# Performance work log

Measured on AMD Instinct MI355X. Metric: run time of the kernel, lower is better.

## Reference

```python
import jax, jax.numpy as jnp
import numpy as np

B, C, H, W = 4, 256, 64, 64
C8 = C // 8  # q/k projection dim = 32

def setup_inputs() -> dict:
    key = jax.random.key(0)
    ks = jax.random.split(key, 6)
    s = 0.02
    return {
        "x": jax.random.normal(ks[0], (B, C, H, W), dtype=jnp.float32),
        "wq": jax.random.normal(ks[1], (C8, C), dtype=jnp.float32) * s,
        "bq": jnp.zeros((C8,), dtype=jnp.float32),
        "wk": jax.random.normal(ks[2], (C8, C), dtype=jnp.float32) * s,
        "bk": jnp.zeros((C8,), dtype=jnp.float32),
        "wv": jax.random.normal(ks[3], (C, C), dtype=jnp.float32) * s,
        "bv": jnp.zeros((C,), dtype=jnp.float32),
        "wo": jax.random.normal(ks[4], (C, C), dtype=jnp.float32) * s,
        "bo": jnp.zeros((C,), dtype=jnp.float32),
        "scale": jnp.zeros((1,), dtype=jnp.float32),
    }

def reference(x, wq, bq, wk, bk, wv, bv, wo, bo, scale):
    b, c, h, w = x.shape
    n = h * w
    xf = x.reshape(b, c, n)  # (B, C, N)
    # 1x1 convs are channel-mixing GEMMs
    q = jnp.einsum('oc,bcn->bon', wq, xf) + bq[None, :, None]  # (B, C8, N)
    k = jnp.einsum('oc,bcn->bon', wk, xf) + bk[None, :, None]  # (B, C8, N)
    v = jnp.einsum('oc,bcn->bon', wv, xf) + bv[None, :, None]  # (B, C,  N)
    inv_sqrt = 1.0 / jnp.sqrt(jnp.asarray(c // 8, dtype=x.dtype))
    scores = jnp.einsum('bon,bom->bnm', q, k) * inv_sqrt  # (B, N, N): query n, key m
    attn = jax.nn.softmax(scores, axis=-1)
    # torch: bmm(value, attn^T) -> attended[:, :, n] = sum_m v[:, :, m] * attn[n, m]
    attended = jnp.einsum('bcm,bnm->bcn', v, attn)  # (B, C, N)
    out = jnp.einsum('oc,bcn->bon', wo, attended) + bo[None, :, None]
    out = out.reshape(b, c, h, w)
    return x + scale[0] * out
```

## Files before the change

kernel.cpp:

```cpp
#include <hip/hip_runtime.h>
#include <stdint.h>

#define B_ 4
#define C_ 256
#define C8_ 32
#define N_ 4096
#define LOG2E 1.4426950408889634f
#define INV_SQRT32 0.17677669529663689f
#define QSCALE (INV_SQRT32 * LOG2E)

typedef __bf16 bf16x8 __attribute__((ext_vector_type(8)));
typedef float f32x16 __attribute__((ext_vector_type(16)));
typedef unsigned int uint4v __attribute__((ext_vector_type(4)));

__device__ __forceinline__ uint16_t f2bf(float f) {
  uint32_t u = __builtin_bit_cast(uint32_t, f);
  return (uint16_t)((u + 0x7FFFu + ((u >> 16) & 1u)) >> 16);
}
__device__ __forceinline__ uint32_t pack2bf(float a, float b) {
  uint32_t ua = __builtin_bit_cast(uint32_t, a);
  uint32_t ub = __builtin_bit_cast(uint32_t, b);
  ua = (ua + 0x7FFFu + ((ua >> 16) & 1u)) >> 16;
  ub = (ub + 0x7FFFu + ((ub >> 16) & 1u)) & 0xFFFF0000u;
  return ua | ub;
}
__device__ __forceinline__ bf16x8 load_bf8(const uint16_t* p) {
  uint4v u = *(const uint4v*)p;
  return __builtin_bit_cast(bf16x8, u);
}
__device__ __forceinline__ f32x16 mfma32(bf16x8 a, bf16x8 b, f32x16 c) {
  return __builtin_amdgcn_mfma_f32_32x32x16_bf16(a, b, c, 0, 0, 0);
}
__device__ __forceinline__ f32x16 mfma32_f8(long a, long b, f32x16 c) {
  return __builtin_amdgcn_mfma_f32_32x32x16_fp8_fp8(a, b, c, 0, 0, 0);
}
__device__ __forceinline__ long u2l(uint2 u) {
  return (long)(((uint64_t)u.y << 32) | u.x);
}

__global__ void k_wcast(const float* __restrict__ wq, const float* __restrict__ wk,
                        const float* __restrict__ wv, const float* __restrict__ wo,
                        uint16_t* __restrict__ wqb, uint16_t* __restrict__ wkb,
                        uint16_t* __restrict__ wvb, uint16_t* __restrict__ wob) {
  int i = blockIdx.x * 256 + threadIdx.x;
  if (i < 8192) {
    int o = i >> 8, c = i & 255;
    wqb[((size_t)(c >> 3) * 32 + o) * 8 + (c & 7)] = f2bf(wq[i]);
  } else if (i < 16384) {
    int j = i - 8192; int o = j >> 8, c = j & 255;
    wkb[((size_t)(c >> 3) * 32 + o) * 8 + (c & 7)] = f2bf(wk[j]);
  } else if (i < 81920) {
    int j = i - 16384; int o = j >> 8, c = j & 255;
    wvb[((size_t)(c >> 3) * 256 + o) * 8 + (c & 7)] = f2bf(wv[j]);
  } else {
    int j = i - 81920; int o = j >> 8, c = j & 255;
    wob[((size_t)(c >> 3) * 256 + o) * 8 + (c & 7)] = f2bf(wo[j]);
  }
}

__global__ __launch_bounds__(320) void k_proj_qkv(
    const float* __restrict__ x,
    const uint16_t* __restrict__ wqb, const float* __restrict__ bq,
    const uint16_t* __restrict__ wkb, const float* __restrict__ bk,
    const uint16_t* __restrict__ wvb, const float* __restrict__ bv,
    uint16_t* __restrict__ Qb, uint16_t* __restrict__ Kt, uint8_t* __restrict__ V8) {
  __shared__ uint4v xTv[32 * 32];
  int b = blockIdx.y >> 1;
  int half = blockIdx.y & 1;
  int n0 = blockIdx.x * 32;
  int tid = threadIdx.x;
  uint16_t* xT = (uint16_t*)xTv;

  if (tid < 256) {
    int r = tid >> 3;
    int l4 = (tid & 7) * 4;
#pragma unroll
    for (int p = 0; p < 8; p++) {
      int c = p * 32 + r;
      float4 v = *(const float4*)(x + ((size_t)b * C_ + c) * N_ + n0 + l4);
      int cg = c >> 3, cj = c & 7;
      xT[(cg * 32 + l4 + 0) * 8 + cj] = f2bf(v.x);
      xT[(cg * 32 + l4 + 1) * 8 + cj] = f2bf(v.y);
      xT[(cg * 32 + l4 + 2) * 8 + cj] = f2bf(v.z);
      xT[(cg * 32 + l4 + 3) * 8 + cj] = f2bf(v.w);
    }
  }
  __syncthreads();

  int wave = tid >> 6;
  int lane = tid & 63;
  int h = lane >> 5, ln = lane & 31;

  if (wave == 0 && half == 0) {
    f32x16 aq;
#pragma unroll
    for (int i = 0; i < 16; i++) aq[i] = 0.0f;
#pragma unroll 4
    for (int c = 0; c < C_; c += 16) {
      bf16x8 bb = __builtin_bit_cast(bf16x8, xTv[(c / 8 + h) * 32 + ln]);
      aq = mfma32(load_bf8(wqb + ((size_t)(c / 8 + h) * 32 + ln) * 8), bb, aq);
    }
#pragma unroll
    for (int g = 0; g < 4; g++) {
      int row = g * 8 + h * 4;
      uint2 pq;
      pq.x = pack2bf((aq[4 * g + 0] + bq[row + 0]) * QSCALE,
                     (aq[4 * g + 1] + bq[row + 1]) * QSCALE);
      pq.y = pack2bf((aq[4 * g + 2] + bq[row + 2]) * QSCALE,
                     (aq[4 * g + 3] + bq[row + 3]) * QSCALE);
      *(uint2*)(Qb + ((size_t)b * N_ + n0 + ln) * C8_ + row) = pq;
    }
  } else if (wave == 0) {
    f32x16 ak;
#pragma unroll
    for (int i = 0; i < 16; i++) ak[i] = 0.0f;
#pragma unroll 4
    for (int c = 0; c < C_; c += 16) {
      bf16x8 bb = __builtin_bit_cast(bf16x8, xTv[(c / 8 + h) * 32 + ln]);
      ak = mfma32(load_bf8(wkb + ((size_t)(c / 8 + h) * 32 + ln) * 8), bb, ak);
    }
#pragma unroll
    for (int g = 0; g < 4; g++) {
      int row = g * 8 + h * 4;
      uint2 pk;
      pk.x = pack2bf(ak[4 * g + 0] + bk[row + 0], ak[4 * g + 1] + bk[row + 1]);
      pk.y = pack2bf(ak[4 * g + 2] + bk[row + 2], ak[4 * g + 3] + bk[row + 3]);
      *(uint2*)(Kt + ((size_t)(b * 4 + g) * N_ + n0 + ln) * 8 + h * 4) = pk;
    }
  } else {
    int o0 = half * 128 + (wave - 1) * 32;
    int och = o0 + ln;
    f32x16 a0;
#pragma unroll
    for (int i = 0; i < 16; i++) a0[i] = 0.0f;
#pragma unroll 4
    for (int c = 0; c < C_; c += 16) {
      bf16x8 xa = __builtin_bit_cast(bf16x8, xTv[(c / 8 + h) * 32 + ln]);
      a0 = mfma32(xa, load_bf8(wvb + ((size_t)(c / 8 + h) * 256 + och) * 8), a0);
    }
    float b0v = bv[och];
    size_t kgb = (size_t)(b * 512 + (n0 >> 3));
#pragma unroll
    for (int g = 0; g < 4; ++g) {
      uint32_t w0 = __builtin_amdgcn_cvt_pk_fp8_f32(a0[4 * g + 0] + b0v,
                                                    a0[4 * g + 1] + b0v, 0, false);
      w0 = __builtin_amdgcn_cvt_pk_fp8_f32(a0[4 * g + 2] + b0v,
                                           a0[4 * g + 3] + b0v, w0, true);
      *(uint32_t*)(V8 + ((kgb + g) * 256 + och) * 8 + 4 * h) = w0;
    }
  }
}

__global__ __launch_bounds__(512, 4) void k_attn(
    const uint16_t* __restrict__ Qb, const uint16_t* __restrict__ Kt,
    const uint8_t* __restrict__ V8, const uint16_t* __restrict__ Wob,
    const float* __restrict__ bo, const float* __restrict__ x,
    const float* __restrict__ scale, float* __restrict__ out) {
  __shared__ uint32_t Pl[2][2048];
  __shared__ uint4v aTv[32 * 32];
  __shared__ float sl[8][32];

  int bx = blockIdx.x;
  int b = bx >> 1;
  int qt = blockIdx.y + 64 * (bx & 1);
  int wave = threadIdx.x >> 6;
  int lane = threadIdx.x & 63;
  int h = lane >> 5, ln = lane & 31;
  int qi = qt * 32 + ln;

  const uint16_t* qrow = Qb + ((size_t)b * N_ + qi) * C8_;
  bf16x8 qf1 = load_bf8(qrow + h * 8);
  bf16x8 qf2 = load_bf8(qrow + 16 + h * 8);
  const uint16_t* k1base = Kt + ((size_t)(b * 4 + h) * N_) * 8;
  const uint16_t* k2base = Kt + ((size_t)(b * 4 + 2 + h) * N_) * 8;

  int o0 = wave * 32;
  const uint8_t* vbase =
      V8 + (size_t)(b * 512) * 2048 + (size_t)h * 2048 + (size_t)(o0 + ln) * 8;

  f32x16 O;
#pragma unroll
  for (int r = 0; r < 16; r++) O[r] = 0.0f;
  float lsum = 0.0f;

  const int K0 = wave * 32;
  bf16x8 ka1 = load_bf8(k1base + (size_t)(K0 + ln) * 8);
  bf16x8 ka2 = load_bf8(k2base + (size_t)(K0 + ln) * 8);

  for (int c = 0; c < 16; ++c) {
    int kbn = ((c + 1) & 15) * 256 + K0;
    bf16x8 kn1 = load_bf8(k1base + (size_t)(kbn + ln) * 8);
    bf16x8 kn2 = load_bf8(k2base + (size_t)(kbn + ln) * 8);

    f32x16 S;
#pragma unroll
    for (int i = 0; i < 16; i++) S[i] = 0.0f;
    S = mfma32(ka1, qf1, S);
    S = mfma32(ka2, qf2, S);

    float P[16];
#pragma unroll
    for (int r = 0; r < 16; r++) P[r] = __builtin_amdgcn_exp2f(fminf(S[r], 7.5f));
    float l0 = 0.0f, l1 = 0.0f;
#pragma unroll
    for (int r = 0; r < 8; r++) { l0 += P[r]; l1 += P[r + 8]; }
    lsum += l0 + l1;

    uint32_t w0 = __builtin_amdgcn_cvt_pk_fp8_f32(P[0], P[1], 0, false);
    w0 = __builtin_amdgcn_cvt_pk_fp8_f32(P[2], P[3], w0, true);
    uint32_t w1 = __builtin_amdgcn_cvt_pk_fp8_f32(P[4], P[5], 0, false);
    w1 = __builtin_amdgcn_cvt_pk_fp8_f32(P[6], P[7], w1, true);
    uint32_t w2 = __builtin_amdgcn_cvt_pk_fp8_f32(P[8], P[9], 0, false);
    w2 = __builtin_amdgcn_cvt_pk_fp8_f32(P[10], P[11], w2, true);
    uint32_t w3 = __builtin_amdgcn_cvt_pk_fp8_f32(P[12], P[13], 0, false);
    w3 = __builtin_amdgcn_cvt_pk_fp8_f32(P[14], P[15], w3, true);
    uint32_t* pw = &Pl[c & 1][wave * 256 + ln * 2 + h];
    pw[0] = w0; pw[64] = w1; pw[128] = w2; pw[192] = w3;

    __syncthreads();

    const uint8_t* vp = vbase + (size_t)c * 65536;
    const uint32_t* pb = &Pl[c & 1][h * 64 + ln * 2];
    __builtin_amdgcn_s_setprio(1);
#pragma unroll 4
    for (int g = 0; g < 16; ++g) {
      uint2 u1 = *(const uint2*)(vp + (size_t)g * 4096);
      uint2 pu = *(const uint2*)(pb + g * 128);
      O = mfma32_f8(u2l(u1), u2l(pu), O);
    }
    __builtin_amdgcn_s_setprio(0);
    ka1 = kn1; ka2 = kn2;
  }

  lsum += __shfl_xor(lsum, 32, 64);
  if (h == 0) sl[wave][ln] = lsum;
  __syncthreads();
  float lg = 0.0f;
#pragma unroll
  for (int w = 0; w < 8; w++) lg += sl[w][ln];
  float inv = 1.0f / lg;
  uint2* aT2 = (uint2*)aTv;
#pragma unroll
  for (int g = 0; g < 4; ++g) {
    uint2 pr2;
    pr2.x = pack2bf(O[4 * g + 0] * inv, O[4 * g + 1] * inv);
    pr2.y = pack2bf(O[4 * g + 2] * inv, O[4 * g + 3] * inv);
    aT2[((wave * 4 + g) * 32 + ln) * 2 + h] = pr2;
  }
  __syncthreads();

  f32x16 acc;
#pragma unroll
  for (int i = 0; i < 16; i++) acc[i] = 0.0f;
#pragma unroll 4
  for (int cc = 0; cc < C_; cc += 16) {
    bf16x8 a = load_bf8(Wob + ((size_t)(cc / 8 + h) * 256 + o0 + ln) * 8);
    bf16x8 bb = __builtin_bit_cast(bf16x8, aTv[(cc / 8 + h) * 32 + ln]);
    acc = mfma32(a, bb, acc);
  }
  float s = scale[0];
#pragma unroll
  for (int r = 0; r < 16; r++) {
    int row = (r & 3) + 8 * (r >> 2) + 4 * h;
    int o = o0 + row;
    size_t idx = ((size_t)b * C_ + o) * N_ + qi;
    out[idx] = x[idx] + s * (acc[r] + bo[o]);
  }
}

extern "C" void kernel_launch(void* const* d_in, const int* in_sizes, int n_in,
                              void* d_out, int out_size, void* d_ws, size_t ws_size,
                              hipStream_t stream) {
  const float* x  = (const float*)d_in[0];
  const float* wq = (const float*)d_in[1];
  const float* bq = (const float*)d_in[2];
  const float* wk = (const float*)d_in[3];
  const float* bk = (const float*)d_in[4];
  const float* wv = (const float*)d_in[5];
  const float* bv = (const float*)d_in[6];
  const float* wo = (const float*)d_in[7];
  const float* bo = (const float*)d_in[8];
  const float* scale = (const float*)d_in[9];
  float* out = (float*)d_out;

  char* w = (char*)d_ws;
  uint16_t* Qb  = (uint16_t*)(w);
  uint16_t* Kt  = (uint16_t*)(w + (1u << 20));
  uint8_t*  V8  = (uint8_t*)(w + (2u << 20));
  uint16_t* Wqb = (uint16_t*)(w + (6u << 20));
  uint16_t* Wkb = Wqb + 32 * 256;
  uint16_t* Wvb = Wkb + 32 * 256;
  uint16_t* Wob = Wvb + 256 * 256;

  k_wcast<<<576, 256, 0, stream>>>(wq, wk, wv, wo, Wqb, Wkb, Wvb, Wob);
  k_proj_qkv<<<dim3(N_ / 32, B_ * 2), 320, 0, stream>>>(x, Wqb, bq, Wkb, bk,
                                                        Wvb, bv, Qb, Kt, V8);
  k_attn<<<dim3(8, 64), 512, 0, stream>>>(Qb, Kt, V8, Wob, bo, x, scale, out);
}
```

Before: 143.7 us.

## Use scaled 32x32x64 FP8 MFMA for PV with re-laid V and swizzled LDS

Replaces the sixteen 32x32x16 FP8 MFMAs per key chunk in the P·V product with four MX-scaled 32x32x64 f8f6f4 MFMAs, using unit scales (0x7F). To feed the wider K dimension, V is written in a new layout with 32 contiguous keys per channel, and the probability tile in LDS is stored per query row with an XOR swizzle so each lane reads 32 bytes. The aim is to cut MFMA issue count and memory instruction count, and to avoid LDS bank conflicts. The risk lies in the operand layout of the scaled instruction and in the swizzle and indexing being correct.

After: 133.5 us, median of 3. 1.08x faster.

```diff
diff --git a/kernel.cpp b/kernel.cpp
--- a/kernel.cpp
+++ b/kernel.cpp
@@ -12,6 +12,7 @@
 typedef __bf16 bf16x8 __attribute__((ext_vector_type(8)));
 typedef float f32x16 __attribute__((ext_vector_type(16)));
 typedef unsigned int uint4v __attribute__((ext_vector_type(4)));
+typedef int i32x8 __attribute__((ext_vector_type(8)));
 
 __device__ __forceinline__ uint16_t f2bf(float f) {
   uint32_t u = __builtin_bit_cast(uint32_t, f);
@@ -31,11 +32,15 @@
 __device__ __forceinline__ f32x16 mfma32(bf16x8 a, bf16x8 b, f32x16 c) {
   return __builtin_amdgcn_mfma_f32_32x32x16_bf16(a, b, c, 0, 0, 0);
 }
-__device__ __forceinline__ f32x16 mfma32_f8(long a, long b, f32x16 c) {
-  return __builtin_amdgcn_mfma_f32_32x32x16_fp8_fp8(a, b, c, 0, 0, 0);
-}
-__device__ __forceinline__ long u2l(uint2 u) {
-  return (long)(((uint64_t)u.y << 32) | u.x);
+__device__ __forceinline__ f32x16 mfma_sc64(i32x8 a, i32x8 b, f32x16 c) {
+  return __builtin_amdgcn_mfma_scale_f32_32x32x64_f8f6f4(
+      a, b, c, 0, 0, 0, 0x7F7F7F7F, 0, 0x7F7F7F7F);
+}
+__device__ __forceinline__ i32x8 pack_i32x8(uint4v lo, uint4v hi) {
+  i32x8 r;
+  r[0] = (int)lo.x; r[1] = (int)lo.y; r[2] = (int)lo.z; r[3] = (int)lo.w;
+  r[4] = (int)hi.x; r[5] = (int)hi.y; r[6] = (int)hi.z; r[7] = (int)hi.w;
+  return r;
 }
 
 __global__ void k_wcast(const float* __restrict__ wq, const float* __restrict__ wk,
@@ -139,14 +144,14 @@
       a0 = mfma32(xa, load_bf8(wvb + ((size_t)(c / 8 + h) * 256 + och) * 8), a0);
     }
     float b0v = bv[och];
-    size_t kgb = (size_t)(b * 512 + (n0 >> 3));
+    uint8_t* vrun = V8 + (((size_t)(b * 128 + (n0 >> 5)) * 256 + och) * 32);
 #pragma unroll
     for (int g = 0; g < 4; ++g) {
       uint32_t w0 = __builtin_amdgcn_cvt_pk_fp8_f32(a0[4 * g + 0] + b0v,
                                                     a0[4 * g + 1] + b0v, 0, false);
       w0 = __builtin_amdgcn_cvt_pk_fp8_f32(a0[4 * g + 2] + b0v,
                                            a0[4 * g + 3] + b0v, w0, true);
-      *(uint32_t*)(V8 + ((kgb + g) * 256 + och) * 8 + 4 * h) = w0;
+      *(uint32_t*)(vrun + 8 * g + 4 * h) = w0;
     }
   }
 }
@@ -156,7 +161,7 @@
     const uint8_t* __restrict__ V8, const uint16_t* __restrict__ Wob,
     const float* __restrict__ bo, const float* __restrict__ x,
     const float* __restrict__ scale, float* __restrict__ out) {
-  __shared__ uint32_t Pl[2][2048];
+  __shared__ uint4v PlV[2][512];
   __shared__ uint4v aTv[32 * 32];
   __shared__ float sl[8][32];
 
@@ -167,6 +172,7 @@
   int lane = threadIdx.x & 63;
   int h = lane >> 5, ln = lane & 31;
   int qi = qt * 32 + ln;
+  uint32_t sw = (uint32_t)(ln & 7) << 4;
 
   const uint16_t* qrow = Qb + ((size_t)b * N_ + qi) * C8_;
   bf16x8 qf1 = load_bf8(qrow + h * 8);
@@ -176,7 +182,7 @@
 
   int o0 = wave * 32;
   const uint8_t* vbase =
-      V8 + (size_t)(b * 512) * 2048 + (size_t)h * 2048 + (size_t)(o0 + ln) * 8;
+      V8 + (((size_t)(b * 128) * 256 + (o0 + ln)) * 32) + (size_t)h * 8192;
 
   f32x16 O;
 #pragma unroll
@@ -206,27 +212,28 @@
     for (int r = 0; r < 8; r++) { l0 += P[r]; l1 += P[r + 8]; }
     lsum += l0 + l1;
 
-    uint32_t w0 = __builtin_amdgcn_cvt_pk_fp8_f32(P[0], P[1], 0, false);
-    w0 = __builtin_amdgcn_cvt_pk_fp8_f32(P[2], P[3], w0, true);
-    uint32_t w1 = __builtin_amdgcn_cvt_pk_fp8_f32(P[4], P[5], 0, false);
-    w1 = __builtin_amdgcn_cvt_pk_fp8_f32(P[6], P[7], w1, true);
-    uint32_t w2 = __builtin_amdgcn_cvt_pk_fp8_f32(P[8], P[9], 0, false);
-    w2 = __builtin_amdgcn_cvt_pk_fp8_f32(P[10], P[11], w2, true);
-    uint32_t w3 = __builtin_amdgcn_cvt_pk_fp8_f32(P[12], P[13], 0, false);
-    w3 = __builtin_amdgcn_cvt_pk_fp8_f32(P[14], P[15], w3, true);
-    uint32_t* pw = &Pl[c & 1][wave * 256 + ln * 2 + h];
-    pw[0] = w0; pw[64] = w1; pw[128] = w2; pw[192] = w3;
+    uint8_t* pbuf = (uint8_t*)PlV[c & 1];
+#pragma unroll
+    for (int s = 0; s < 4; ++s) {
+      uint32_t w = __builtin_amdgcn_cvt_pk_fp8_f32(P[4 * s + 0], P[4 * s + 1], 0, false);
+      w = __builtin_amdgcn_cvt_pk_fp8_f32(P[4 * s + 2], P[4 * s + 3], w, true);
+      uint32_t off = ((uint32_t)(ln * 256 + K0 + 8 * s + 4 * h)) ^ sw;
+      *(uint32_t*)(pbuf + off) = w;
+    }
 
     __syncthreads();
 
     const uint8_t* vp = vbase + (size_t)c * 65536;
-    const uint32_t* pb = &Pl[c & 1][h * 64 + ln * 2];
+    const uint8_t* pr = (const uint8_t*)PlV[c & 1];
+    uint32_t pb0 = (uint32_t)(ln * 256 + 32 * h);
     __builtin_amdgcn_s_setprio(1);
-#pragma unroll 4
-    for (int g = 0; g < 16; ++g) {
-      uint2 u1 = *(const uint2*)(vp + (size_t)g * 4096);
-      uint2 pu = *(const uint2*)(pb + g * 128);
-      O = mfma32_f8(u2l(u1), u2l(pu), O);
+#pragma unroll
+    for (int t = 0; t < 4; ++t) {
+      uint4v vlo = *(const uint4v*)(vp + (size_t)t * 16384);
+      uint4v vhi = *(const uint4v*)(vp + (size_t)t * 16384 + 16);
+      uint4v plo = *(const uint4v*)(pr + ((pb0 + 64 * t) ^ sw));
+      uint4v phi = *(const uint4v*)(pr + ((pb0 + 64 * t + 16) ^ sw));
+      O = mfma_sc64(pack_i32x8(vlo, vhi), pack_i32x8(plo, phi), O);
     }
     __builtin_amdgcn_s_setprio(0);
     ka1 = kn1; ka2 = kn2;
```
